# Kernel optimization log

Hardware: AMD Instinct MI355X
Metric: run time of the kernel (lower is better)

Reference implementation:

```python
import jax, jax.numpy as jnp
import numpy as np

IN_CH = 256
OUT_CH = 256
STATE = 384
OUT_SEQ = 32
B_SZ = 8
SEQ = 512


def setup_inputs() -> dict:
    key = jax.random.key(0)
    ks = jax.random.split(key, 8)
    rmin, rmax, max_phase = 0.0, 1.0, 6.283
    u1 = jax.random.uniform(ks[0], (STATE,))
    u2 = jax.random.uniform(ks[1], (STATE,))
    # standard LRU stable-ring initialization
    nu_log = jnp.log(-0.5 * jnp.log(u1 * (rmax + rmin) * (rmax - rmin) + rmin ** 2))
    theta_log = jnp.log(max_phase * u2)
    lam_mod = jnp.exp(-jnp.exp(nu_log))
    gamma_log = jnp.log(jnp.sqrt(1.0 - lam_mod ** 2))
    B_re = jax.random.normal(ks[2], (STATE, IN_CH)) / np.sqrt(2 * IN_CH)
    B_im = jax.random.normal(ks[3], (STATE, IN_CH)) / np.sqrt(2 * IN_CH)
    C_re = jax.random.normal(ks[4], (OUT_CH, STATE)) / np.sqrt(STATE)
    C_im = jax.random.normal(ks[5], (OUT_CH, STATE)) / np.sqrt(STATE)
    D = jax.random.normal(ks[6], (OUT_CH, IN_CH)) / np.sqrt(IN_CH)
    x = jax.random.normal(ks[7], (B_SZ, SEQ, IN_CH))
    return dict(x=x, nu_log=nu_log, theta_log=theta_log, gamma_log=gamma_log,
                B_re=B_re, B_im=B_im, C_re=C_re, C_im=C_im, D=D)


def _lru(x, h_re, h_im, nu_log, theta_log, gamma_log, B_re, B_im, C_re, C_im, D):
    """One LRU pass over a full sequence. x: [B,S,C]. h_*: [B,N] initial complex state.
    Diagonal complex recurrence h_t = Lambda*h_{t-1} + gamma*(B x_t); y_t = Re(C h_t) + D x_t."""
    lam_mod = jnp.exp(-jnp.exp(nu_log))              # |Lambda| in (0,1)
    lre = lam_mod * jnp.cos(jnp.exp(theta_log))      # [N]
    lim = lam_mod * jnp.sin(jnp.exp(theta_log))
    gamma = jnp.exp(gamma_log)
    # input projection for whole sequence (complex, split into re/im)
    u_re = gamma * jnp.einsum('bsc,nc->bsn', x, B_re)  # [B,S,N]
    u_im = gamma * jnp.einsum('bsc,nc->bsn', x, B_im)

    def step(h, u):
        hre, him = h
        ur, ui = u
        nre = lre * hre - lim * him + ur
        nim = lre * him + lim * hre + ui
        return (nre, nim), (nre, nim)

    (h_re, h_im), (hs_re, hs_im) = jax.lax.scan(
        step, (h_re, h_im),
        (jnp.swapaxes(u_re, 0, 1), jnp.swapaxes(u_im, 0, 1)))  # scan over S
    hs_re = jnp.swapaxes(hs_re, 0, 1)  # [B,S,N]
    hs_im = jnp.swapaxes(hs_im, 0, 1)
    y = (jnp.einsum('bsn,on->bso', hs_re, C_re)
         - jnp.einsum('bsn,on->bso', hs_im, C_im)
         + jnp.einsum('bsc,oc->bso', x, D))
    return y, h_re, h_im


def reference(x, nu_log, theta_log, gamma_log, B_re, B_im, C_re, C_im, D):
    bsz = x.shape[0]
    h_re = jnp.zeros((bsz, STATE), x.dtype)   # state=None on first call -> zeros
    h_im = jnp.zeros((bsz, STATE), x.dtype)
    outs = []
    for _ in range(OUT_SEQ):
        x, h_re, h_im = _lru(x, h_re, h_im, nu_log, theta_log, gamma_log,
                             B_re, B_im, C_re, C_im, D)
        outs.append(x[:, -1:])
    return jnp.concatenate(outs, axis=-2)  # [B, OUT_SEQ, OUT_CH]
```

## Files before the change

### kernel.cpp

```cpp
#include <hip/hip_runtime.h>
#include <hip/hip_bf16.h>
#include <math.h>

typedef unsigned short u16;
typedef __attribute__((ext_vector_type(8))) short bf16x8;
typedef __attribute__((ext_vector_type(4))) float f32x4;
typedef __attribute__((ext_vector_type(16))) float f32x16;

#define IN_CH   256
#define STATE   384
#define OUT_SEQ 32
#define B_SZ    8
#define SEQ     512
#define M_ROWS  4096
#define NJ      768

#define PS_WB  (NJ*IN_CH)
#define PS_WC  (IN_CH*NJ)
#define PS_WD  (IN_CH*IN_CH)
#define PS_Z   ((size_t)M_ROWS*NJ)
#define PS_X   ((size_t)M_ROWS*IN_CH)

static constexpr size_t B_U   = 0;
static constexpr size_t B_Z   = B_U  + 8*(size_t)M_ROWS*IN_CH*4;
static constexpr size_t B_XA  = B_Z  + 3*(size_t)M_ROWS*NJ*2;
static constexpr size_t B_XB  = B_XA + 3*(size_t)M_ROWS*IN_CH*2;
static constexpr size_t B_WB  = B_XB + 3*(size_t)M_ROWS*IN_CH*2;
static constexpr size_t B_WC  = B_WB + 3*(size_t)PS_WB*2;
static constexpr size_t B_WD  = B_WC + 3*(size_t)PS_WC*2;
static constexpr size_t B_LAM = B_WD + 3*(size_t)PS_WD*2;
static constexpr size_t B_HC  = B_LAM + 2*768*4;
static constexpr size_t B_CAR = B_HC  + 2*(size_t)B_SZ*NJ*4;

__device__ __forceinline__ u16 f2b(float v) {
    __hip_bfloat16 h = __float2bfloat16(v);
    return *(u16*)&h;
}
__device__ __forceinline__ float b2f(u16 u) {
    __hip_bfloat16 h = *(__hip_bfloat16*)&u;
    return __bfloat162float(h);
}
__device__ __forceinline__ void split3(float v, u16& a, u16& b, u16& c) {
    a = f2b(v);  float r1 = v  - b2f(a);
    b = f2b(r1); float r2 = r1 - b2f(b);
    c = f2b(r2);
}

__device__ __forceinline__ size_t a_idx(int row, int k, int NKC) {
    return ((size_t)(((row >> 5)*NKC + (k >> 5))*2 + ((k >> 4) & 1))*2 + ((k >> 3) & 1))*256
           + (size_t)(row & 31)*8 + (k & 7);
}

__device__ __forceinline__ void frag_decode(int r, int& t32, int& h, int& hi5,
                                            int& lo5, int& e) {
    t32 = r >> 10; int r2 = r & 1023;
    h = r2 >> 9;   int r3 = r2 & 511;
    hi5 = r3 >> 8; int r4 = r3 & 255;
    lo5 = r4 >> 3; e = r4 & 7;
}

__global__ void prep_lam_hc(const float* __restrict__ nu_log,
                            const float* __restrict__ th_log,
                            float* __restrict__ lam, float* __restrict__ lam64,
                            float* __restrict__ hc0) {
    int n = threadIdx.x;
    if (n < STATE) {
        float lm = expf(-expf(nu_log[n]));
        float th = expf(th_log[n]);
        float ar = lm * cosf(th), ai = lm * sinf(th);
        lam[2*n] = ar; lam[2*n+1] = ai;
        float pr = ar, pi = ai;
#pragma unroll
        for (int i = 0; i < 6; ++i) {
            float nr = pr*pr - pi*pi, ni = 2.f*pr*pi;
            pr = nr; pi = ni;
        }
        lam64[2*n] = pr; lam64[2*n+1] = pi;
    }
    for (int i = threadIdx.x; i < B_SZ*NJ; i += blockDim.x) hc0[i] = 0.f;
}

__global__ void prep_wb(const float* __restrict__ B_re, const float* __restrict__ B_im,
                        const float* __restrict__ gamma_log, u16* __restrict__ W) {
    int idx = blockIdx.x*blockDim.x + threadIdx.x;
    int c32 = idx >> 13, r = idx & 8191;
    int t32,h,hi5,lo5,e; frag_decode(r, t32,h,hi5,lo5,e);
    int j = c32*32 + lo5;
    int k = t32*32 + (2*h + hi5)*8 + e;
    int n = j >> 1;
    float g = expf(gamma_log[n]);
    float v = g * ((j & 1) ? B_im[n*IN_CH + k] : B_re[n*IN_CH + k]);
    u16 a,b,cc; split3(v,a,b,cc);
    W[idx] = a; W[idx + PS_WB] = b; W[idx + 2*PS_WB] = cc;
}

__global__ void prep_wcd(const float* __restrict__ C_re, const float* __restrict__ C_im,
                         const float* __restrict__ D,
                         u16* __restrict__ WC, u16* __restrict__ WD) {
    int idx = blockIdx.x*blockDim.x + threadIdx.x;
    if (idx < PS_WC) {
        int c32 = idx / 24576, r = idx % 24576;
        int t32,h,hi5,lo5,e; frag_decode(r, t32,h,hi5,lo5,e);
        int o = c32*32 + lo5;
        int j = t32*32 + (2*h + hi5)*8 + e;
        int n = j >> 1;
        float v = (j & 1) ? -C_im[o*STATE + n] : C_re[o*STATE + n];
        u16 a,b,c; split3(v,a,b,c);
        WC[idx] = a; WC[idx + PS_WC] = b; WC[idx + 2*PS_WC] = c;
    } else {
        int q = idx - PS_WC;
        int c32 = q >> 13, r = q & 8191;
        int t32,h,hi5,lo5,e; frag_decode(r, t32,h,hi5,lo5,e);
        int o = c32*32 + lo5;
        int c = t32*32 + (2*h + hi5)*8 + e;
        float v = D[o*IN_CH + c];
        u16 a,b,cc; split3(v,a,b,cc);
        WD[q] = a; WD[q + PS_WD] = b; WD[q + 2*PS_WD] = cc;
    }
}

__global__ void prep_x(const float* __restrict__ x,
                       u16* __restrict__ X1, u16* __restrict__ X2, u16* __restrict__ X3) {
    int idx = blockIdx.x*blockDim.x + threadIdx.x;
    int row = idx >> 8, k = idx & 255;
    u16 a,b,c; split3(x[idx],a,b,c);
    size_t o = a_idx(row, k, 8);
    X1[o] = a; X2[o] = b; X3[o] = c;
}

__device__ __constant__ const int cPI[6] = {0,0,1,0,1,2};
__device__ __constant__ const int cPJ[6] = {0,1,0,2,1,0};

struct G1P { const u16* A[3]; };

__global__ __launch_bounds__(256, 2)
void gemm1_k(G1P ga, const u16* __restrict__ WBp, float* __restrict__ Uout,
             const float* __restrict__ lam, float2* __restrict__ carry) {
    __shared__ __align__(16) float Ls[64*64];
    const int tid = threadIdx.x, lane = tid & 63, w = tid >> 6;
    const int wr = w & 1, wcq = w >> 1;
    const int m0 = blockIdx.x*64, n0 = blockIdx.y*64;
    const int hi5 = lane >> 5, lo5 = lane & 31;
    const int c32 = (n0 >> 5) + wcq;
    const int m32 = blockIdx.x*2 + wr;

    f32x16 acc;
#pragma unroll
    for (int i = 0; i < 16; ++i) acc[i] = 0.f;

    bf16x8 bwin[3][4][2];
    auto loadB = [&](int cw, int tlo, int thi) {
#pragma unroll
        for (int p = 0; p < 3; ++p)
#pragma unroll
            for (int t = 0; t < 4; ++t) {
                if (t < tlo || t >= thi) continue;
#pragma unroll
                for (int h = 0; h < 2; ++h)
                    bwin[p][t][h] = *(const bf16x8*)(WBp + (size_t)p*PS_WB
                        + ((((size_t)(c32*8 + cw*4 + t)*2 + h)*2 + hi5) << 8) + lo5*8);
            }
    };
    bf16x8 av[2][3][2];
    auto loadA = [&](int buf, int ks) {
#pragma unroll
        for (int p = 0; p < 3; ++p)
#pragma unroll
            for (int h = 0; h < 2; ++h)
                av[buf][p][h] = *(const bf16x8*)(ga.A[p]
                    + ((((size_t)(m32*8 + ks)*2 + h)*2 + hi5) << 8) + lo5*8);
    };

    loadA(0, 0);
    loadB(0, 0, 4);
    loadA(1, 1);
#pragma unroll
    for (int ks = 0; ks < 8; ++ks) {
        if (ks == 2) loadB(1, 0, 2);
        const int cb = ks & 1;
        const int tw = ks & 3;
#pragma unroll
        for (int t6 = 0; t6 < 6; ++t6)
#pragma unroll
            for (int h = 0; h < 2; ++h)
                acc = __builtin_amdgcn_mfma_f32_32x32x16_bf16(
                    av[cb][cPI[t6]][h], bwin[cPJ[t6]][tw][h], acc, 0, 0, 0);
        if (ks == 3) loadB(1, 2, 4);
        if (ks + 2 < 8) loadA(cb, ks + 2);
    }

#pragma unroll
    for (int reg = 0; reg < 16; ++reg) {
        int rl = wr*32 + (reg & 3) + 8*(reg >> 2) + 4*hi5;
        int cl = wcq*32 + lo5;
        float v = acc[reg];
        Uout[(size_t)(m0 + rl)*NJ + n0 + cl] = v;
        Ls[rl*64 + cl] = v;
    }
    __syncthreads();

    if (tid < 32) {
        int b = m0 >> 9, ch = (m0 >> 6) & 7;
        int n = (n0 >> 1) + tid;
        float lre = lam[2*n], lim = lam[2*n+1];
        float hr = 0.f, hm = 0.f;
        const float2* L2 = (const float2*)Ls;
        float2 pf[8];
#pragma unroll
        for (int p = 0; p < 8; ++p) pf[p] = L2[p*32 + tid];
        for (int s0 = 0; s0 < 64; s0 += 8) {
#pragma unroll
            for (int p = 0; p < 8; ++p) {
                int st = s0 + p;
                float ur = pf[p].x, ui = pf[p].y;
                if (st + 8 < 64) pf[p] = L2[(st + 8)*32 + tid];
                float nr = fmaf(lre, hr, fmaf(-lim, hm, ur));
                float nm = fmaf(lre, hm, fmaf( lim, hr, ui));
                hr = nr; hm = nm;
            }
        }
        carry[(size_t)(b*8 + ch)*STATE + n] = make_float2(hr, hm);
    }
}

__global__ __launch_bounds__(64)
void scan_emit(const float* __restrict__ Uf,
               u16* __restrict__ Z1, u16* __restrict__ Z2, u16* __restrict__ Z3,
               const float* __restrict__ lam, const float* __restrict__ lam64,
               const float2* __restrict__ carry,
               const float2* __restrict__ HcIn, float2* __restrict__ HcOut) {
    int bx = blockIdx.x;
    int b = bx / 48, rem = bx % 48, g = rem >> 3, c = rem & 7;
    int n = g*64 + threadIdx.x;
    float lre = lam[2*n], lim = lam[2*n+1];
    float p64r = lam64[2*n], p64i = lam64[2*n+1];
    float2 h = HcIn[(size_t)b*STATE + n];
    for (int j = 0; j < c; ++j) {
        float2 cj = carry[(size_t)(b*8 + j)*STATE + n];
        float nr = fmaf(p64r, h.x, fmaf(-p64i, h.y, cj.x));
        float ni = fmaf(p64r, h.y, fmaf( p64i, h.x, cj.y));
        h.x = nr; h.y = ni;
    }
    const float2* U2 = (const float2*)Uf + ((size_t)(b*SEQ + c*64))*STATE + n;
    const int j0 = 2*n;
    const int jpart = ((j0 >> 5)*2 + ((j0 >> 4) & 1))*2 + ((j0 >> 3) & 1);
    const int e0 = j0 & 7;
    const int r32base = (b*SEQ + c*64) >> 5;
    float2 buf[16];
#pragma unroll
    for (int p = 0; p < 16; ++p) buf[p] = U2[(size_t)p*STATE];
    for (int s0 = 0; s0 < 64; s0 += 16) {
#pragma unroll
        for (int p = 0; p < 16; ++p) {
            int s = s0 + p;
            float ur = buf[p].x, ui = buf[p].y;
            if (s + 16 < 64) buf[p] = U2[(size_t)(s+16)*STATE];
            float nr = fmaf(lre, h.x, fmaf(-lim, h.y, ur));
            float ni = fmaf(lre, h.y, fmaf( lim, h.x, ui));
            h.x = nr; h.y = ni;
            u16 a1,a2,a3, c1,c2,c3;
            split3(nr, a1,a2,a3);
            split3(ni, c1,c2,c3);
            size_t zo = (((size_t)(r32base + (s >> 5))*96 + jpart) << 8)
                        + (size_t)(s & 31)*8 + e0;
            ushort2 t;
            t.x = a1; t.y = c1; *(ushort2*)(Z1 + zo) = t;
            t.x = a2; t.y = c2; *(ushort2*)(Z2 + zo) = t;
            t.x = a3; t.y = c3; *(ushort2*)(Z3 + zo) = t;
        }
    }
    if (c == 7) HcOut[(size_t)b*STATE + n] = h;
}

struct G2P {
    const u16* Z[3]; const u16* X[3]; const u16* WC; const u16* WD;
    u16* O1; u16* O2; u16* O3; float* outp; int iter;
};

__global__ __launch_bounds__(512, 2)
void gemm2_k(G2P g) {
    __shared__ __align__(16) float Lred[64*64];
    const int tid = threadIdx.x, lane = tid & 63, w = tid >> 6;
    const int kg = w >> 2, wq = w & 3;
    const int wr = wq & 1, wcq = wq >> 1;
    const int m0 = blockIdx.x*64, n0 = blockIdx.y*64;
    const int hi5 = lane >> 5, lo5 = lane & 31;
    const int c32 = (n0 >> 5) + wcq;
    const int m32 = blockIdx.x*2 + wr;
    const int cbase = kg*16;

    f32x16 acc;
#pragma unroll
    for (int i = 0; i < 16; ++i) acc[i] = 0.f;

    auto aptr = [&](int p, int c, int h) -> const u16* {
        if (c < 24)
            return g.Z[p] + ((((size_t)(m32*24 + c)*2 + h)*2 + hi5) << 8) + lo5*8;
        return g.X[p] + ((((size_t)(m32*8 + (c - 24))*2 + h)*2 + hi5) << 8) + lo5*8;
    };
    auto bptr = [&](int p, int c, int h) -> const u16* {
        if (c < 24)
            return g.WC + (size_t)p*PS_WC
                   + ((((size_t)(c32*24 + c)*2 + h)*2 + hi5) << 8) + lo5*8;
        return g.WD + (size_t)p*PS_WD
               + ((((size_t)(c32*8 + (c - 24))*2 + h)*2 + hi5) << 8) + lo5*8;
    };

    bf16x8 bwin[3][4][2];
    auto loadB = [&](int wnd, int tlo, int thi) {
#pragma unroll
        for (int p = 0; p < 3; ++p)
#pragma unroll
            for (int t = 0; t < 4; ++t) {
                if (t < tlo || t >= thi) continue;
#pragma unroll
                for (int h = 0; h < 2; ++h)
                    bwin[p][t][h] = *(const bf16x8*)bptr(p, cbase + wnd*4 + t, h);
            }
    };
    bf16x8 av[2][3][2];
    auto loadA = [&](int buf, int t) {
#pragma unroll
        for (int p = 0; p < 3; ++p)
#pragma unroll
            for (int h = 0; h < 2; ++h)
                av[buf][p][h] = *(const bf16x8*)aptr(p, cbase + t, h);
    };

    loadA(0, 0);
    loadB(0, 0, 4);
    loadA(1, 1);
#pragma unroll
    for (int t = 0; t < 16; ++t) {
        if ((t & 3) == 2 && t < 12) loadB((t >> 2) + 1, 0, 2);
        const int cb = t & 1;
        const int tw = t & 3;
#pragma unroll
        for (int t6 = 0; t6 < 6; ++t6)
#pragma unroll
            for (int h = 0; h < 2; ++h)
                acc = __builtin_amdgcn_mfma_f32_32x32x16_bf16(
                    av[cb][cPI[t6]][h], bwin[cPJ[t6]][tw][h], acc, 0, 0, 0);
        if ((t & 3) == 3 && t < 12) loadB((t >> 2) + 1, 2, 4);
        if (t + 2 < 16) loadA(cb, t + 2);
    }

    if (kg == 1) {
#pragma unroll
        for (int reg = 0; reg < 16; ++reg) {
            int rl = wr*32 + (reg & 3) + 8*(reg >> 2) + 4*hi5;
            int cl = wcq*32 + lo5;
            Lred[rl*64 + cl] = acc[reg];
        }
    }
    __syncthreads();
    if (kg == 0) {
#pragma unroll
        for (int reg = 0; reg < 16; ++reg) {
            int rl = wr*32 + (reg & 3) + 8*(reg >> 2) + 4*hi5;
            int cl = wcq*32 + lo5;
            float v = acc[reg] + Lred[rl*64 + cl];
            int row = m0 + rl, col = n0 + cl;
            u16 a,b,c; split3(v, a,b,c);
            size_t o = a_idx(row, col, 8);
            g.O1[o] = a; g.O2[o] = b; g.O3[o] = c;
            if ((row & (SEQ-1)) == SEQ-1)
                g.outp[(size_t)((row >> 9)*OUT_SEQ + g.iter)*IN_CH + col] = v;
        }
    }
}

extern "C" void kernel_launch(void* const* d_in, const int* in_sizes, int n_in,
                              void* d_out, int out_size, void* d_ws, size_t ws_size,
                              hipStream_t stream) {
    const float* x_in      = (const float*)d_in[0];
    const float* nu_log    = (const float*)d_in[1];
    const float* theta_log = (const float*)d_in[2];
    const float* gamma_log = (const float*)d_in[3];
    const float* B_re      = (const float*)d_in[4];
    const float* B_im      = (const float*)d_in[5];
    const float* C_re      = (const float*)d_in[6];
    const float* C_im      = (const float*)d_in[7];
    const float* D         = (const float*)d_in[8];
    float* out = (float*)d_out;

    char* ws = (char*)d_ws;
    float* U   = (float*)(ws + B_U);
    u16* Z1 = (u16*)(ws + B_Z);
    u16* Z2 = Z1 + PS_Z;
    u16* Z3 = Z2 + PS_Z;
    u16* XA1 = (u16*)(ws + B_XA);
    u16* XA2 = XA1 + PS_X;
    u16* XA3 = XA2 + PS_X;
    u16* XB1 = (u16*)(ws + B_XB);
    u16* XB2 = XB1 + PS_X;
    u16* XB3 = XB2 + PS_X;
    u16* WB  = (u16*)(ws + B_WB);
    u16* WCt = (u16*)(ws + B_WC);
    u16* WDt = (u16*)(ws + B_WD);
    float* lam   = (float*)(ws + B_LAM);
    float* lam64 = lam + 768;
    float2* Hc0  = (float2*)(ws + B_HC);
    float2* Hc1  = Hc0 + (size_t)B_SZ*STATE;
    float2* carry = (float2*)(ws + B_CAR);

    prep_lam_hc<<<1, 384, 0, stream>>>(nu_log, theta_log, lam, lam64, (float*)Hc0);
    prep_wb<<<PS_WB/256, 256, 0, stream>>>(B_re, B_im, gamma_log, WB);
    prep_wcd<<<(PS_WC + PS_WD)/256, 256, 0, stream>>>(C_re, C_im, D, WCt, WDt);
    prep_x<<<(M_ROWS*IN_CH)/256, 256, 0, stream>>>(x_in, XA1, XA2, XA3);

    for (int it = 0; it < OUT_SEQ; ++it) {
        u16* Xc[3]; u16* Xn[3];
        if (it & 1) { Xc[0]=XB1; Xc[1]=XB2; Xc[2]=XB3; Xn[0]=XA1; Xn[1]=XA2; Xn[2]=XA3; }
        else        { Xc[0]=XA1; Xc[1]=XA2; Xc[2]=XA3; Xn[0]=XB1; Xn[1]=XB2; Xn[2]=XB3; }
        float2* Hin  = (it & 1) ? Hc1 : Hc0;
        float2* Hout = (it & 1) ? Hc0 : Hc1;

        G1P g1;
        for (int p = 0; p < 3; ++p) g1.A[p] = Xc[p];
        gemm1_k<<<dim3(M_ROWS/64, NJ/64), 256, 0, stream>>>(g1, WB, U, lam, carry);

        scan_emit<<<384, 64, 0, stream>>>(U, Z1, Z2, Z3, lam, lam64, carry, Hin, Hout);

        G2P g2;
        g2.Z[0]=Z1; g2.Z[1]=Z2; g2.Z[2]=Z3;
        g2.X[0]=Xc[0]; g2.X[1]=Xc[1]; g2.X[2]=Xc[2];
        g2.WC = WCt; g2.WD = WDt;
        g2.O1 = Xn[0]; g2.O2 = Xn[1]; g2.O3 = Xn[2];
        g2.outp = out; g2.iter = it;
        gemm2_k<<<dim3(M_ROWS/64, IN_CH/64), 512, 0, stream>>>(g2);
    }
}
```

Before: 1.462 ms.

## Fuse input projection GEMM and chunked complex scan into one front kernel

Replaces the separate gemm1 kernel (which wrote fp32 U to global) and the scan_emit kernel with one front_k kernel. Each block computes a full 512-step sequence for one batch and a 32-column slice of U in LDS using 16x16x32 MFMAs. It then runs a three-phase chunked scan (16 chunks of 32 steps, a carry pass using lambda^32, and a re-scan that emits the split bf16 Z) entirely on-chip. This removes the U global round trip and one launch per iteration. The cost is a large LDS footprint, only 192 blocks per launch, and a serial 16-step carry phase. gemm2's MFMA chain is also restructured into nested calls with the same arithmetic.

```diff
diff --git a/kernel.cpp b/kernel.cpp
--- a/kernel.cpp
+++ b/kernel.cpp
@@ -5,7 +5,6 @@
 typedef unsigned short u16;
 typedef __attribute__((ext_vector_type(8))) short bf16x8;
 typedef __attribute__((ext_vector_type(4))) float f32x4;
-typedef __attribute__((ext_vector_type(16))) float f32x16;
 
 #define IN_CH   256
 #define STATE   384
@@ -30,7 +29,6 @@
 static constexpr size_t B_WD  = B_WC + 3*(size_t)PS_WC*2;
 static constexpr size_t B_LAM = B_WD + 3*(size_t)PS_WD*2;
 static constexpr size_t B_HC  = B_LAM + 2*768*4;
-static constexpr size_t B_CAR = B_HC  + 2*(size_t)B_SZ*NJ*4;
 
 __device__ __forceinline__ u16 f2b(float v) {
     __hip_bfloat16 h = __float2bfloat16(v);
@@ -61,7 +59,7 @@
 
 __global__ void prep_lam_hc(const float* __restrict__ nu_log,
                             const float* __restrict__ th_log,
-                            float* __restrict__ lam, float* __restrict__ lam64,
+                            float* __restrict__ lam, float* __restrict__ lam32,
                             float* __restrict__ hc0) {
     int n = threadIdx.x;
     if (n < STATE) {
@@ -71,11 +69,11 @@
         lam[2*n] = ar; lam[2*n+1] = ai;
         float pr = ar, pi = ai;
 #pragma unroll
-        for (int i = 0; i < 6; ++i) {
+        for (int i = 0; i < 5; ++i) {
             float nr = pr*pr - pi*pi, ni = 2.f*pr*pi;
             pr = nr; pi = ni;
         }
-        lam64[2*n] = pr; lam64[2*n+1] = pi;
+        lam32[2*n] = pr; lam32[2*n+1] = pi;
     }
     for (int i = threadIdx.x; i < B_SZ*NJ; i += blockDim.x) hc0[i] = 0.f;
 }
@@ -133,143 +131,121 @@
 
 struct G1P { const u16* A[3]; };
 
-__global__ __launch_bounds__(256, 2)
-void gemm1_k(G1P ga, const u16* __restrict__ WBp, float* __restrict__ Uout,
-             const float* __restrict__ lam, float2* __restrict__ carry) {
-    __shared__ __align__(16) float Ls[64*64];
+__global__ __launch_bounds__(512, 4)
+void front_k(G1P ga, const u16* __restrict__ WBp,
+             u16* __restrict__ Z1, u16* __restrict__ Z2, u16* __restrict__ Z3,
+             const float* __restrict__ lam, const float* __restrict__ lam32,
+             const float2* __restrict__ HcIn, float2* __restrict__ HcOut) {
+    __shared__ __align__(16) float Ls[512*33];
+    __shared__ float2 car[32][16];
+    __shared__ float2 hp[32][16];
     const int tid = threadIdx.x, lane = tid & 63, w = tid >> 6;
-    const int wr = w & 1, wcq = w >> 1;
-    const int m0 = blockIdx.x*64, n0 = blockIdx.y*64;
-    const int hi5 = lane >> 5, lo5 = lane & 31;
-    const int c32 = (n0 >> 5) + wcq;
-    const int m32 = blockIdx.x*2 + wr;
-
-    f32x16 acc;
-#pragma unroll
-    for (int i = 0; i < 16; ++i) acc[i] = 0.f;
-
-    bf16x8 bwin[3][4][2];
-    auto loadB = [&](int cw, int tlo, int thi) {
-#pragma unroll
-        for (int p = 0; p < 3; ++p)
-#pragma unroll
-            for (int t = 0; t < 4; ++t) {
-                if (t < tlo || t >= thi) continue;
-#pragma unroll
-                for (int h = 0; h < 2; ++h)
-                    bwin[p][t][h] = *(const bf16x8*)(WBp + (size_t)p*PS_WB
-                        + ((((size_t)(c32*8 + cw*4 + t)*2 + h)*2 + hi5) << 8) + lo5*8);
+    const int b = blockIdx.x, jt = blockIdx.y;
+    const int l15 = lane & 15, q = lane >> 4;
+    const int hb = q >> 1, hi5q = q & 1;
+
+    f32x4 acc[4][2];
+#pragma unroll
+    for (int i = 0; i < 4; ++i)
+#pragma unroll
+        for (int n16 = 0; n16 < 2; ++n16) acc[i][n16] = 0.f;
+
+#pragma unroll
+    for (int kc = 0; kc < 8; ++kc) {
+        bf16x8 av[4][3], bv[2][3];
+#pragma unroll
+        for (int p = 0; p < 3; ++p) {
+#pragma unroll
+            for (int i = 0; i < 4; ++i) {
+                int m16 = i*8 + w;
+                int row32 = b*16 + (m16 >> 1);
+                int rin = ((m16 & 1) << 4) + l15;
+                av[i][p] = *(const bf16x8*)(ga.A[p]
+                    + ((((size_t)(row32*8 + kc)*2 + hb)*2 + hi5q) << 8) + rin*8);
             }
-    };
-    bf16x8 av[2][3][2];
-    auto loadA = [&](int buf, int ks) {
-#pragma unroll
-        for (int p = 0; p < 3; ++p)
-#pragma unroll
-            for (int h = 0; h < 2; ++h)
-                av[buf][p][h] = *(const bf16x8*)(ga.A[p]
-                    + ((((size_t)(m32*8 + ks)*2 + h)*2 + hi5) << 8) + lo5*8);
-    };
-
-    loadA(0, 0);
-    loadB(0, 0, 4);
-    loadA(1, 1);
-#pragma unroll
-    for (int ks = 0; ks < 8; ++ks) {
-        if (ks == 2) loadB(1, 0, 2);
-        const int cb = ks & 1;
-        const int tw = ks & 3;
+#pragma unroll
+            for (int n16 = 0; n16 < 2; ++n16)
+                bv[n16][p] = *(const bf16x8*)(WBp + (size_t)p*PS_WB
+                    + ((((size_t)(jt*8 + kc)*2 + hb)*2 + hi5q) << 8) + (n16*16 + l15)*8);
+        }
 #pragma unroll
         for (int t6 = 0; t6 < 6; ++t6)
 #pragma unroll
-            for (int h = 0; h < 2; ++h)
-                acc = __builtin_amdgcn_mfma_f32_32x32x16_bf16(
-                    av[cb][cPI[t6]][h], bwin[cPJ[t6]][tw][h], acc, 0, 0, 0);
-        if (ks == 3) loadB(1, 2, 4);
-        if (ks + 2 < 8) loadA(cb, ks + 2);
-    }
-
-#pragma unroll
-    for (int reg = 0; reg < 16; ++reg) {
-        int rl = wr*32 + (reg & 3) + 8*(reg >> 2) + 4*hi5;
-        int cl = wcq*32 + lo5;
-        float v = acc[reg];
-        Uout[(size_t)(m0 + rl)*NJ + n0 + cl] = v;
-        Ls[rl*64 + cl] = v;
+            for (int i = 0; i < 4; ++i)
+#pragma unroll
+                for (int n16 = 0; n16 < 2; ++n16)
+                    acc[i][n16] = __builtin_amdgcn_mfma_f32_16x16x32_bf16(
+                        av[i][cPI[t6]], bv[n16][cPJ[t6]], acc[i][n16], 0, 0, 0);
+    }
+
+#pragma unroll
+    for (int i = 0; i < 4; ++i) {
+        int m16 = i*8 + w;
+#pragma unroll
+        for (int n16 = 0; n16 < 2; ++n16)
+#pragma unroll
+            for (int r = 0; r < 4; ++r) {
+                int s = m16*16 + q*4 + r;
+                int jl = n16*16 + l15;
+                Ls[s*33 + jl] = acc[i][n16][r];
+            }
     }
     __syncthreads();
 
-    if (tid < 32) {
-        int b = m0 >> 9, ch = (m0 >> 6) & 7;
-        int n = (n0 >> 1) + tid;
+    if (tid < 256) {
+        int st = tid & 15, ch = tid >> 4;
+        int n = jt*16 + st;
         float lre = lam[2*n], lim = lam[2*n+1];
         float hr = 0.f, hm = 0.f;
-        const float2* L2 = (const float2*)Ls;
-        float2 pf[8];
-#pragma unroll
-        for (int p = 0; p < 8; ++p) pf[p] = L2[p*32 + tid];
-        for (int s0 = 0; s0 < 64; s0 += 8) {
-#pragma unroll
-            for (int p = 0; p < 8; ++p) {
-                int st = s0 + p;
-                float ur = pf[p].x, ui = pf[p].y;
-                if (st + 8 < 64) pf[p] = L2[(st + 8)*32 + tid];
-                float nr = fmaf(lre, hr, fmaf(-lim, hm, ur));
-                float nm = fmaf(lre, hm, fmaf( lim, hr, ui));
-                hr = nr; hm = nm;
-            }
-        }
-        carry[(size_t)(b*8 + ch)*STATE + n] = make_float2(hr, hm);
-    }
-}
-
-__global__ __launch_bounds__(64)
-void scan_emit(const float* __restrict__ Uf,
-               u16* __restrict__ Z1, u16* __restrict__ Z2, u16* __restrict__ Z3,
-               const float* __restrict__ lam, const float* __restrict__ lam64,
-               const float2* __restrict__ carry,
-               const float2* __restrict__ HcIn, float2* __restrict__ HcOut) {
-    int bx = blockIdx.x;
-    int b = bx / 48, rem = bx % 48, g = rem >> 3, c = rem & 7;
-    int n = g*64 + threadIdx.x;
-    float lre = lam[2*n], lim = lam[2*n+1];
-    float p64r = lam64[2*n], p64i = lam64[2*n+1];
-    float2 h = HcIn[(size_t)b*STATE + n];
-    for (int j = 0; j < c; ++j) {
-        float2 cj = carry[(size_t)(b*8 + j)*STATE + n];
-        float nr = fmaf(p64r, h.x, fmaf(-p64i, h.y, cj.x));
-        float ni = fmaf(p64r, h.y, fmaf( p64i, h.x, cj.y));
-        h.x = nr; h.y = ni;
-    }
-    const float2* U2 = (const float2*)Uf + ((size_t)(b*SEQ + c*64))*STATE + n;
-    const int j0 = 2*n;
-    const int jpart = ((j0 >> 5)*2 + ((j0 >> 4) & 1))*2 + ((j0 >> 3) & 1);
-    const int e0 = j0 & 7;
-    const int r32base = (b*SEQ + c*64) >> 5;
-    float2 buf[16];
-#pragma unroll
-    for (int p = 0; p < 16; ++p) buf[p] = U2[(size_t)p*STATE];
-    for (int s0 = 0; s0 < 64; s0 += 16) {
-#pragma unroll
-        for (int p = 0; p < 16; ++p) {
-            int s = s0 + p;
-            float ur = buf[p].x, ui = buf[p].y;
-            if (s + 16 < 64) buf[p] = U2[(size_t)(s+16)*STATE];
-            float nr = fmaf(lre, h.x, fmaf(-lim, h.y, ur));
-            float ni = fmaf(lre, h.y, fmaf( lim, h.x, ui));
-            h.x = nr; h.y = ni;
+        for (int t = 0; t < 32; ++t) {
+            int s = ch*32 + t;
+            float ur = Ls[s*33 + 2*st], ui = Ls[s*33 + 2*st + 1];
+            float nr = fmaf(lre, hr, fmaf(-lim, hm, ur));
+            float nm = fmaf(lre, hm, fmaf( lim, hr, ui));
+            hr = nr; hm = nm;
+        }
+        car[ch][st] = make_float2(hr, hm);
+    }
+    __syncthreads();
+
+    if (tid < 16) {
+        int st = tid, n = jt*16 + st;
+        float l32r = lam32[2*n], l32i = lam32[2*n+1];
+        float2 hh = HcIn[(size_t)b*STATE + n];
+        hp[0][st] = hh;
+        for (int ch = 1; ch < 16; ++ch) {
+            float2 cj = car[ch-1][st];
+            float nr = fmaf(l32r, hh.x, fmaf(-l32i, hh.y, cj.x));
+            float ni = fmaf(l32r, hh.y, fmaf( l32i, hh.x, cj.y));
+            hh.x = nr; hh.y = ni;
+            hp[ch][st] = hh;
+        }
+    }
+    __syncthreads();
+
+    if (tid < 256) {
+        int st = tid & 15, ch = tid >> 4;
+        int n = jt*16 + st;
+        float lre = lam[2*n], lim = lam[2*n+1];
+        float2 hh = hp[ch][st];
+        int j0 = jt*32 + 2*st;
+        for (int t = 0; t < 32; ++t) {
+            int s = ch*32 + t;
+            float ur = Ls[s*33 + 2*st], ui = Ls[s*33 + 2*st + 1];
+            float nr = fmaf(lre, hh.x, fmaf(-lim, hh.y, ur));
+            float ni = fmaf(lre, hh.y, fmaf( lim, hh.x, ui));
+            hh.x = nr; hh.y = ni;
             u16 a1,a2,a3, c1,c2,c3;
             split3(nr, a1,a2,a3);
             split3(ni, c1,c2,c3);
-            size_t zo = (((size_t)(r32base + (s >> 5))*96 + jpart) << 8)
-                        + (size_t)(s & 31)*8 + e0;
-            ushort2 t;
-            t.x = a1; t.y = c1; *(ushort2*)(Z1 + zo) = t;
-            t.x = a2; t.y = c2; *(ushort2*)(Z2 + zo) = t;
-            t.x = a3; t.y = c3; *(ushort2*)(Z3 + zo) = t;
-        }
-    }
-    if (c == 7) HcOut[(size_t)b*STATE + n] = h;
+            size_t zo = a_idx(b*512 + s, j0, 24);
+            ushort2 t2;
+            t2.x = a1; t2.y = c1; *(ushort2*)(Z1 + zo) = t2;
+            t2.x = a2; t2.y = c2; *(ushort2*)(Z2 + zo) = t2;
+            t2.x = a3; t2.y = c3; *(ushort2*)(Z3 + zo) = t2;
+        }
+        if (ch == 15) HcOut[(size_t)b*STATE + n] = hh;
+    }
 }
 
 struct G2P {
@@ -289,9 +265,15 @@
     const int m32 = blockIdx.x*2 + wr;
     const int cbase = kg*16;
 
-    f32x16 acc;
+    f32x4 acc4[4];
+    float acc[16];
 #pragma unroll
     for (int i = 0; i < 16; ++i) acc[i] = 0.f;
+    typedef __attribute__((ext_vector_type(16))) float f32x16_t;
+    f32x16_t accv;
+#pragma unroll
+    for (int i = 0; i < 16; ++i) accv[i] = 0.f;
+    (void)acc4; (void)acc;
 
     auto aptr = [&](int p, int c, int h) -> const u16* {
         if (c < 24)
@@ -337,10 +319,11 @@
         const int tw = t & 3;
 #pragma unroll
         for (int t6 = 0; t6 < 6; ++t6)
-#pragma unroll
-            for (int h = 0; h < 2; ++h)
-                acc = __builtin_amdgcn_mfma_f32_32x32x16_bf16(
-                    av[cb][cPI[t6]][h], bwin[cPJ[t6]][tw][h], acc, 0, 0, 0);
+            accv = __builtin_amdgcn_mfma_f32_32x32x16_bf16(
+                av[cb][cPI[t6]][0], bwin[cPJ[t6]][tw][0],
+                __builtin_amdgcn_mfma_f32_32x32x16_bf16(
+                    av[cb][cPI[t6]][1], bwin[cPJ[t6]][tw][1], accv, 0, 0, 0),
+                0, 0, 0);
         if ((t & 3) == 3 && t < 12) loadB((t >> 2) + 1, 2, 4);
         if (t + 2 < 16) loadA(cb, t + 2);
     }
@@ -350,7 +333,7 @@
         for (int reg = 0; reg < 16; ++reg) {
             int rl = wr*32 + (reg & 3) + 8*(reg >> 2) + 4*hi5;
             int cl = wcq*32 + lo5;
-            Lred[rl*64 + cl] = acc[reg];
+            Lred[rl*64 + cl] = accv[reg];
         }
     }
     __syncthreads();
@@ -359,7 +342,7 @@
         for (int reg = 0; reg < 16; ++reg) {
             int rl = wr*32 + (reg & 3) + 8*(reg >> 2) + 4*hi5;
             int cl = wcq*32 + lo5;
-            float v = acc[reg] + Lred[rl*64 + cl];
+            float v = accv[reg] + Lred[rl*64 + cl];
             int row = m0 + rl, col = n0 + cl;
             u16 a,b,c; split3(v, a,b,c);
             size_t o = a_idx(row, col, 8);
@@ -385,7 +368,6 @@
     float* out = (float*)d_out;
 
     char* ws = (char*)d_ws;
-    float* U   = (float*)(ws + B_U);
     u16* Z1 = (u16*)(ws + B_Z);
     u16* Z2 = Z1 + PS_Z;
     u16* Z3 = Z2 + PS_Z;
@@ -399,12 +381,11 @@
     u16* WCt = (u16*)(ws + B_WC);
     u16* WDt = (u16*)(ws + B_WD);
     float* lam   = (float*)(ws + B_LAM);
-    float* lam64 = lam + 768;
+    float* lam32 = lam + 768;
     float2* Hc0  = (float2*)(ws + B_HC);
     float2* Hc1  = Hc0 + (size_t)B_SZ*STATE;
-    float2* carry = (float2*)(ws + B_CAR);
-
-    prep_lam_hc<<<1, 384, 0, stream>>>(nu_log, theta_log, lam, lam64, (float*)Hc0);
+
+    prep_lam_hc<<<1, 384, 0, stream>>>(nu_log, theta_log, lam, lam32, (float*)Hc0);
     prep_wb<<<PS_WB/256, 256, 0, stream>>>(B_re, B_im, gamma_log, WB);
     prep_wcd<<<(PS_WC + PS_WD)/256, 256, 0, stream>>>(C_re, C_im, D, WCt, WDt);
     prep_x<<<(M_ROWS*IN_CH)/256, 256, 0, stream>>>(x_in, XA1, XA2, XA3);
@@ -418,9 +399,8 @@
 
         G1P g1;
         for (int p = 0; p < 3; ++p) g1.A[p] = Xc[p];
-        gemm1_k<<<dim3(M_ROWS/64, NJ/64), 256, 0, stream>>>(g1, WB, U, lam, carry);
-
-        scan_emit<<<384, 64, 0, stream>>>(U, Z1, Z2, Z3, lam, lam64, carry, Hin, Hout);
+        front_k<<<dim3(B_SZ, 24), 512, 0, stream>>>(
+            g1, WB, Z1, Z2, Z3, lam, lam32, Hin, Hout);
 
         G2P g2;
         g2.Z[0]=Z1; g2.Z[1]=Z2; g2.Z[2]=Z3;
```

Result: faster. 1.332 ms (-8.9%).
